# Performance work log

Measured on AMD Instinct MI355X. Metric: run time of the kernel, lower is better.

## Reference

```python
import jax, jax.numpy as jnp
import numpy as np
import math

D_MODEL = 512
EXPAND = 2
D_INNER = EXPAND * D_MODEL          # 1024
HEADDIM = 16
NHEADS = D_INNER // HEADDIM         # 64
NGROUPS = 1
D_STATE = 16
D_CONV = 4
CHUNK = 256
CONV_DIM = D_INNER + 2 * NGROUPS * D_STATE      # 1056
D_IN_PROJ = 2 * D_INNER + 2 * NGROUPS * D_STATE + NHEADS  # 2144
EPS = 1e-5


def setup_inputs() -> dict:
    key = jax.random.key(0)
    ks = jax.random.split(key, 9)
    B, L = 2, 4096
    u = jax.random.normal(ks[0], (B, L, D_MODEL), dtype=jnp.float32)
    in_proj_w = jax.random.normal(ks[1], (D_IN_PROJ, D_MODEL), dtype=jnp.float32) * (1.0 / math.sqrt(D_MODEL))
    conv_w = jax.random.normal(ks[2], (CONV_DIM, D_CONV), dtype=jnp.float32) * (1.0 / math.sqrt(D_CONV))
    conv_b = jnp.zeros((CONV_DIM,), dtype=jnp.float32)
    # dt_bias = inverse-softplus of dt sampled log-uniform in [1e-3, 1e-1]
    dt = jnp.exp(jax.random.uniform(ks[3], (NHEADS,)) * (math.log(0.1) - math.log(0.001)) + math.log(0.001))
    dt_bias = dt + jnp.log(-jnp.expm1(-dt))
    A_log = jnp.log(jax.random.uniform(ks[4], (NHEADS,), minval=1.0, maxval=16.0))
    D_skip = jnp.ones((NHEADS,), dtype=jnp.float32)
    norm_w = jnp.ones((D_INNER,), dtype=jnp.float32)
    out_proj_w = jax.random.normal(ks[5], (D_MODEL, D_INNER), dtype=jnp.float32) * (1.0 / math.sqrt(D_INNER))
    return {"u": u, "in_proj_w": in_proj_w, "conv_w": conv_w, "conv_b": conv_b,
            "dt_bias": dt_bias, "A_log": A_log, "D_skip": D_skip,
            "norm_w": norm_w, "out_proj_w": out_proj_w}


def _segsum(x):
    # x: (..., T) -> (..., T, T) lower-triangular cumulative segment sums
    T = x.shape[-1]
    cs = jnp.cumsum(x, axis=-1)
    s = cs[..., :, None] - cs[..., None, :]
    mask = jnp.tril(jnp.ones((T, T), dtype=bool))
    return jnp.where(mask, s, -jnp.inf)


def _ssd(xdt, dA, Bm, Cm):
    # xdt: (b,l,h,p) already multiplied by dt; dA: (b,l,h); Bm,Cm: (b,l,h,n)
    b, l, h, p = xdt.shape
    n = Bm.shape[-1]
    nc = l // CHUNK
    xr = xdt.reshape(b, nc, CHUNK, h, p)
    Br = Bm.reshape(b, nc, CHUNK, h, n)
    Cr = Cm.reshape(b, nc, CHUNK, h, n)
    dAr = dA.reshape(b, nc, CHUNK, h).transpose(0, 3, 1, 2)  # (b,h,nc,c)
    A_cs = jnp.cumsum(dAr, axis=-1)
    # intra-chunk (diagonal blocks)
    Ldec = jnp.exp(_segsum(dAr))                              # (b,h,nc,c,c)
    Y_diag = jnp.einsum('bclhn,bcshn,bhcls,bcshp->bclhp', Cr, Br, Ldec, xr)
    # per-chunk final states
    decay_states = jnp.exp(A_cs[..., -1:] - A_cs)             # (b,h,nc,c)
    states = jnp.einsum('bclhn,bhcl,bclhp->bchpn', Br, decay_states, xr)
    states = jnp.concatenate([jnp.zeros_like(states[:, :1]), states], axis=1)
    chunk_sums = jnp.pad(A_cs[..., -1], ((0, 0), (0, 0), (1, 0)))  # (b,h,nc+1)
    decay_chunk = jnp.exp(_segsum(chunk_sums))                # (b,h,nc+1,nc+1)
    new_states = jnp.einsum('bhzc,bchpn->bzhpn', decay_chunk, states)
    prev_states = new_states[:, :-1]                          # (b,nc,h,p,n)
    # inter-chunk contribution
    state_decay_out = jnp.exp(A_cs)                           # (b,h,nc,c)
    Y_off = jnp.einsum('bclhn,bchpn,bhcl->bclhp', Cr, prev_states, state_decay_out)
    return (Y_diag + Y_off).reshape(b, l, h, p)


def _forward(u, in_proj_w, conv_w, conv_b, dt_bias, A_log, D_skip, norm_w, out_proj_w):
    b, l, _ = u.shape
    zxbcdt = jnp.einsum('bld,ed->ble', u, in_proj_w)
    z = zxbcdt[..., :D_INNER]
    xBC = zxbcdt[..., D_INNER:D_INNER + CONV_DIM]
    dt = zxbcdt[..., D_INNER + CONV_DIM:]
    dt = jax.nn.softplus(dt + dt_bias)                        # (b,l,h)
    # causal depthwise conv1d + silu
    xBC_t = xBC.transpose(0, 2, 1)                            # (b, conv_dim, l)
    conv_out = jax.lax.conv_general_dilated(
        xBC_t, conv_w[:, None, :], window_strides=(1,),
        padding=[(D_CONV - 1, 0)], feature_group_count=CONV_DIM,
        dimension_numbers=('NCH', 'OIH', 'NCH'))
    xBC = jax.nn.silu((conv_out + conv_b[None, :, None]).transpose(0, 2, 1))
    x = xBC[..., :D_INNER].reshape(b, l, NHEADS, HEADDIM)
    Bg = xBC[..., D_INNER:D_INNER + NGROUPS * D_STATE].reshape(b, l, NGROUPS, D_STATE)
    Cg = xBC[..., D_INNER + NGROUPS * D_STATE:].reshape(b, l, NGROUPS, D_STATE)
    hpg = NHEADS // NGROUPS
    Bm = jnp.repeat(Bg, hpg, axis=2)                          # (b,l,h,n)
    Cm = jnp.repeat(Cg, hpg, axis=2)
    A = -jnp.exp(A_log)                                       # (h,)
    dA = dt * A                                               # (b,l,h)
    y = _ssd(x * dt[..., None], dA, Bm, Cm)
    y = y + x * D_skip[None, None, :, None]
    y = y.reshape(b, l, D_INNER)
    # gated RMSNorm (norm_before_gate=False): norm(y * silu(z)) * w
    y = y * jax.nn.silu(z)
    y = y * jax.lax.rsqrt(jnp.mean(y * y, axis=-1, keepdims=True) + EPS) * norm_w
    return jnp.einsum('ble,de->bld', y, out_proj_w)


def reference(u, in_proj_w, conv_w, conv_b, dt_bias, A_log, D_skip, norm_w, out_proj_w):
    return _forward(u, in_proj_w, conv_w, conv_b, dt_bias, A_log, D_skip, norm_w, out_proj_w)
```

## Files before the change

kernel.cpp:

```cpp
#include <hip/hip_runtime.h>
#include <hip/hip_bf16.h>
#include <math.h>

#define D_MODEL   512
#define D_INNER   1024
#define NHEADS    64
#define HEADDIM   16
#define D_STATE   16
#define CONV_DIM  1056
#define D_IN_PROJ 2144
#define CHUNK     256
#define NCHUNK    16
#define BATCH     2
#define SEQ       4096
#define ROWS      (BATCH * SEQ)
#define LDZX      2176

typedef __bf16    bf16x8 __attribute__((ext_vector_type(8)));
typedef _Float16  f16x8  __attribute__((ext_vector_type(8)));
typedef float     f32x4  __attribute__((ext_vector_type(4)));
typedef float     f32x16 __attribute__((ext_vector_type(16)));
typedef unsigned short u16x8 __attribute__((ext_vector_type(8)));
typedef unsigned int   u32x4 __attribute__((ext_vector_type(4)));

__device__ __forceinline__ float softplusf(float x) {
    return (x > 20.f) ? x : log1pf(expf(x));
}
__device__ __forceinline__ float siluf(float x) {
    return x / (1.f + expf(-x));
}
__device__ __forceinline__ unsigned short f2b(float x) {
    union { __hip_bfloat16 h; unsigned short u; } cv;
    cv.h = __float2bfloat16(x);
    return cv.u;
}
__device__ __forceinline__ float b2f(unsigned short u) {
    union { float f; unsigned int i; } c;
    c.i = (unsigned int)u << 16;
    return c.f;
}
__device__ __forceinline__ void load_lds16(const unsigned short* g, unsigned short* l) {
    __builtin_amdgcn_global_load_lds(
        (const __attribute__((address_space(1))) void*)g,
        (__attribute__((address_space(3))) void*)l,
        16, 0, 0);
}

__global__ __launch_bounds__(256) void cast_all(const float* __restrict__ u,
                                                const float* __restrict__ Win,
                                                const float* __restrict__ Wout,
                                                unsigned short* __restrict__ u_bf,
                                                unsigned short* __restrict__ win_bf,
                                                unsigned short* __restrict__ wout_bf) {
    const int bid = blockIdx.x;
    u16x8 o;
    if (bid < 2048) {
        const int i = (bid * 256 + threadIdx.x) * 8;
        float4 a = *(const float4*)(u + i);
        float4 b = *(const float4*)(u + i + 4);
        o[0] = f2b(a.x); o[1] = f2b(a.y); o[2] = f2b(a.z); o[3] = f2b(a.w);
        o[4] = f2b(b.x); o[5] = f2b(b.y); o[6] = f2b(b.z); o[7] = f2b(b.w);
        *(u16x8*)(u_bf + i) = o;
    } else if (bid < 2592) {
        const int i = ((bid - 2048) * 256 + threadIdx.x) * 8;
        const int n = 2144 * 512;
        if (i + 8 <= n) {
            float4 a = *(const float4*)(Win + i);
            float4 b = *(const float4*)(Win + i + 4);
            o[0] = f2b(a.x); o[1] = f2b(a.y); o[2] = f2b(a.z); o[3] = f2b(a.w);
            o[4] = f2b(b.x); o[5] = f2b(b.y); o[6] = f2b(b.z); o[7] = f2b(b.w);
        } else {
            #pragma unroll
            for (int j = 0; j < 8; ++j) o[j] = (i + j < n) ? f2b(Win[i + j]) : (unsigned short)0;
        }
        *(u16x8*)(win_bf + i) = o;
    } else {
        const int i = ((bid - 2592) * 256 + threadIdx.x) * 8;
        float4 a = *(const float4*)(Wout + i);
        float4 b = *(const float4*)(Wout + i + 4);
        o[0] = f2b(a.x); o[1] = f2b(a.y); o[2] = f2b(a.z); o[3] = f2b(a.w);
        o[4] = f2b(b.x); o[5] = f2b(b.y); o[6] = f2b(b.z); o[7] = f2b(b.w);
        *(u16x8*)(wout_bf + i) = o;
    }
}

__global__ __launch_bounds__(256) void gemm_in(const unsigned short* __restrict__ A,
                                               const unsigned short* __restrict__ B,
                                               unsigned short* __restrict__ C16,
                                               float* __restrict__ dtsp,
                                               const float* __restrict__ dtb) {
    __shared__ unsigned short smem[32768];
    const int t    = threadIdx.x;
    const int wave = t >> 6;
    const int lane = t & 63;
    const int bid  = blockIdx.x;
    const int swz  = (bid & 7) * 136 + (bid >> 3);
    const int by   = swz / 17;
    const int bx   = swz - by * 17;
    const int bm   = by * 128;
    const int bn   = bx * 128;
    const int wr   = wave >> 1;
    const int wc   = wave & 1;

    const int fr = lane & 15;
    const int kb = (lane >> 4) * 8;

    f32x4 acc[4][4] = {};

    auto stage = [&](int it) {
        const int k0 = it * 64;
        unsigned short* dst = smem + (it & 1) * 16384;
        #pragma unroll
        for (int q = 0; q < 4; ++q) {
            const int p = q * 256 + t;
            const int r = p >> 3;
            const int sl = (p & 7) ^ (r & 7);
            load_lds16(A + (size_t)(bm + r) * 512 + k0 + sl * 8, dst + p * 8);
        }
        #pragma unroll
        for (int q = 0; q < 4; ++q) {
            const int p = q * 256 + t;
            const int r = p >> 3;
            const int sl = (p & 7) ^ (r & 7);
            load_lds16(B + (size_t)(bn + r) * 512 + k0 + sl * 8, dst + 8192 + p * 8);
        }
    };

    stage(0);
    __syncthreads();

    for (int it = 0; it < 8; ++it) {
        if (it + 1 < 8) stage(it + 1);
        const unsigned short* Ab = smem + (it & 1) * 16384;
        const unsigned short* Bb = Ab + 8192;
        #pragma unroll
        for (int kk = 0; kk < 2; ++kk) {
            const int c0 = kk * 32 + kb;
            const int s0 = c0 >> 3;
            bf16x8 af[4], bfr[4];
            #pragma unroll
            for (int m = 0; m < 4; ++m) {
                const int R = wr * 64 + m * 16 + fr;
                af[m] = *reinterpret_cast<const bf16x8*>(&Ab[R * 64 + ((s0 ^ (R & 7)) << 3)]);
            }
            #pragma unroll
            for (int n = 0; n < 4; ++n) {
                const int R = wc * 64 + n * 16 + fr;
                bfr[n] = *reinterpret_cast<const bf16x8*>(&Bb[R * 64 + ((s0 ^ (R & 7)) << 3)]);
            }
            #pragma unroll
            for (int m = 0; m < 4; ++m)
                #pragma unroll
                for (int n = 0; n < 4; ++n)
                    acc[m][n] = __builtin_amdgcn_mfma_f32_16x16x32_bf16(af[m], bfr[n], acc[m][n], 0, 0, 0);
        }
        __syncthreads();
    }

    if (bn == 2048) {
        #pragma unroll
        for (int m = 0; m < 4; ++m) {
            #pragma unroll
            for (int n = 0; n < 4; ++n) {
                const int col = bn + wc * 64 + fr + n * 16;
                if (col >= 2080 && col < 2144) {
                    const int h = col - 2080;
                    const float bias = dtb[h];
                    #pragma unroll
                    for (int j = 0; j < 4; ++j) {
                        const int row = bm + wr * 64 + ((lane >> 4) << 2) + m * 16 + j;
                        dtsp[(size_t)row * 64 + h] = softplusf(acc[m][n][j] + bias);
                    }
                }
            }
        }
    }
    #pragma unroll
    for (int m = 0; m < 4; ++m) {
        #pragma unroll
        for (int n = 0; n < 4; ++n) {
            const int lcol = wc * 64 + fr + n * 16;
            #pragma unroll
            for (int j = 0; j < 4; ++j) {
                const int lrow = wr * 64 + ((lane >> 4) << 2) + m * 16 + j;
                smem[lrow * 128 + lcol] = f2b(acc[m][n][j]);
            }
        }
    }
    __syncthreads();
    #pragma unroll
    for (int p = 0; p < 8; ++p) {
        const int r = p * 16 + (t >> 4);
        const int cl = (t & 15) * 8;
        u16x8 v = *(const u16x8*)&smem[r * 128 + cl];
        *(u16x8*)(C16 + (size_t)(bm + r) * LDZX + bn + cl) = v;
    }
}

__global__ __launch_bounds__(256) void gemm_out(const unsigned short* __restrict__ A,
                                                const unsigned short* __restrict__ B,
                                                float* __restrict__ C) {
    __shared__ unsigned short smem[24576];
    const int t    = threadIdx.x;
    const int wave = t >> 6;
    const int lane = t & 63;
    const int bm   = blockIdx.y * 128;
    const int bn   = blockIdx.x * 64;
    const int wr   = wave >> 1;
    const int wc   = wave & 1;

    const int fr = lane & 15;
    const int kb = (lane >> 4) * 8;

    f32x4 acc[4][2] = {};

    auto stage = [&](int it) {
        const int k0 = it * 64;
        unsigned short* dst = smem + (it & 1) * 12288;
        #pragma unroll
        for (int q = 0; q < 4; ++q) {
            const int p = q * 256 + t;
            const int r = p >> 3;
            const int sl = (p & 7) ^ (r & 7);
            load_lds16(A + (size_t)(bm + r) * 1024 + k0 + sl * 8, dst + p * 8);
        }
        #pragma unroll
        for (int q = 0; q < 2; ++q) {
            const int p = q * 256 + t;
            const int r = p >> 3;
            const int sl = (p & 7) ^ (r & 7);
            load_lds16(B + (size_t)(bn + r) * 1024 + k0 + sl * 8, dst + 8192 + p * 8);
        }
    };

    stage(0);
    __syncthreads();

    for (int it = 0; it < 16; ++it) {
        if (it + 1 < 16) stage(it + 1);
        const unsigned short* Ab = smem + (it & 1) * 12288;
        const unsigned short* Bb = Ab + 8192;
        #pragma unroll
        for (int kk = 0; kk < 2; ++kk) {
            const int c0 = kk * 32 + kb;
            const int s0 = c0 >> 3;
            bf16x8 af[4], bfr[2];
            #pragma unroll
            for (int m = 0; m < 4; ++m) {
                const int R = wr * 64 + m * 16 + fr;
                af[m] = *reinterpret_cast<const bf16x8*>(&Ab[R * 64 + ((s0 ^ (R & 7)) << 3)]);
            }
            #pragma unroll
            for (int n = 0; n < 2; ++n) {
                const int R = wc * 32 + n * 16 + fr;
                bfr[n] = *reinterpret_cast<const bf16x8*>(&Bb[R * 64 + ((s0 ^ (R & 7)) << 3)]);
            }
            #pragma unroll
            for (int m = 0; m < 4; ++m)
                #pragma unroll
                for (int n = 0; n < 2; ++n)
                    acc[m][n] = __builtin_amdgcn_mfma_f32_16x16x32_bf16(af[m], bfr[n], acc[m][n], 0, 0, 0);
        }
        __syncthreads();
    }

    const int cr0 = bm + wr * 64 + ((lane >> 4) << 2);
    const int cc0 = bn + wc * 32 + fr;
    #pragma unroll
    for (int m = 0; m < 4; ++m)
        #pragma unroll
        for (int n = 0; n < 2; ++n)
            #pragma unroll
            for (int j = 0; j < 4; ++j)
                C[(size_t)(cr0 + m * 16 + j) * 512 + cc0 + n * 16] = acc[m][n][j];
}

__global__ void conv_silu44(const unsigned short* __restrict__ zxb, const float* __restrict__ cw,
                            const float* __restrict__ cb, unsigned short* __restrict__ xcb) {
    int idx = blockIdx.x * blockDim.x + threadIdx.x;
    if (idx >= (ROWS / 4) * (CONV_DIM / 4)) return;
    const int cq  = idx % (CONV_DIM / 4);
    const int blq = idx / (CONV_DIM / 4);
    const int bl0 = blq * 4;
    const int l0  = bl0 % SEQ;
    const int c4  = cq * 4;
    const unsigned short* base = zxb + (size_t)bl0 * LDZX + D_INNER + c4;
    float4 w0 = *(const float4*)(cw + (c4 + 0) * 4);
    float4 w1 = *(const float4*)(cw + (c4 + 1) * 4);
    float4 w2 = *(const float4*)(cw + (c4 + 2) * 4);
    float4 w3 = *(const float4*)(cw + (c4 + 3) * 4);
    float4 bb = *(const float4*)(cb + c4);
    float4 in[7];
    #pragma unroll
    for (int k = 0; k < 7; ++k) {
        const int off = k - 3;
        if (l0 == 0 && k < 3) {
            in[k] = make_float4(0.f, 0.f, 0.f, 0.f);
        } else {
            ushort4 uu = *(const ushort4*)(base + (long)off * LDZX);
            in[k] = make_float4(b2f(uu.x), b2f(uu.y), b2f(uu.z), b2f(uu.w));
        }
    }
    #pragma unroll
    for (int r = 0; r < 4; ++r) {
        ushort4 o;
        o.x = f2b(siluf(bb.x + w0.x * in[r].x + w0.y * in[r + 1].x + w0.z * in[r + 2].x + w0.w * in[r + 3].x));
        o.y = f2b(siluf(bb.y + w1.x * in[r].y + w1.y * in[r + 1].y + w1.z * in[r + 2].y + w1.w * in[r + 3].y));
        o.z = f2b(siluf(bb.z + w2.x * in[r].z + w2.y * in[r + 1].z + w2.z * in[r + 2].z + w2.w * in[r + 3].z));
        o.w = f2b(siluf(bb.w + w3.x * in[r].w + w3.y * in[r + 1].w + w3.z * in[r + 2].w + w3.w * in[r + 3].w));
        *(ushort4*)(xcb + (size_t)(bl0 + r) * CONV_DIM + c4) = o;
    }
}

__global__ __launch_bounds__(256, 4) void ssd_chunk(const unsigned short* __restrict__ xcb,
                                                    const float* __restrict__ dtsp,
                                                    const float* __restrict__ A_log,
                                                    unsigned short* __restrict__ ypre16,
                                                    float* __restrict__ states,
                                                    float* __restrict__ csb,
                                                    float* __restrict__ csum) {
    __shared__ _Float16 Bb[256][16];
    __shared__ _Float16 Cb[256][16];
    __shared__ _Float16 Xt[16][264];
    __shared__ _Float16 Bt[16][264];
    __shared__ float csL[256];
    __shared__ __align__(16) _Float16 decL[256];
    __shared__ float wsumL[4];

    const int bid = blockIdx.x;
    const int h = bid & 63;
    const int c = (bid >> 6) & 15;
    const int b = bid >> 10;
    const int t = threadIdx.x;
    const int wv = t >> 6;
    const int lane = t & 63;
    const int fr = lane & 15;
    const int hi = lane >> 4;
    const int l31 = lane & 31;
    const int hi5 = lane >> 5;
    const int row = b * SEQ + c * CHUNK + t;

    float Ah  = -__expf(A_log[h]);
    float dtv = dtsp[(size_t)row * NHEADS + h];
    float val = dtv * Ah;
    #pragma unroll
    for (int off = 1; off < 64; off <<= 1) {
        float o = __shfl_up(val, off, 64);
        if (lane >= off) val += o;
    }
    if (lane == 63) wsumL[wv] = val;
    __syncthreads();
    float pre = 0.f, cl = 0.f;
    #pragma unroll
    for (int w2 = 0; w2 < 4; ++w2) {
        float s = wsumL[w2];
        if (w2 < wv) pre += s;
        cl += s;
    }
    float cst = val + pre;
    csL[t] = cst;
    csb[(size_t)bid * 256 + t] = cst;
    if (t == 0) csum[(b * 64 + h) * 16 + c] = cl;
    decL[t] = (_Float16)__expf(cl - cst);

    const unsigned short* xrow = xcb + (size_t)row * CONV_DIM;
    u16x8 braw0 = *(const u16x8*)(xrow + D_INNER);
    u16x8 braw1 = *(const u16x8*)(xrow + D_INNER + 8);
    u16x8 craw0 = *(const u16x8*)(xrow + D_INNER + D_STATE);
    u16x8 craw1 = *(const u16x8*)(xrow + D_INNER + D_STATE + 8);
    u16x8 xraw0 = *(const u16x8*)(xrow + h * HEADDIM);
    u16x8 xraw1 = *(const u16x8*)(xrow + h * HEADDIM + 8);
    float bv[16], cv[16], xv[16];
    #pragma unroll
    for (int n = 0; n < 8; ++n) {
        bv[n] = b2f(braw0[n]); bv[8 + n] = b2f(braw1[n]);
        cv[n] = b2f(craw0[n]); cv[8 + n] = b2f(craw1[n]);
        xv[n] = b2f(xraw0[n]); xv[8 + n] = b2f(xraw1[n]);
    }
    {
        f16x8 pk;
        #pragma unroll
        for (int n = 0; n < 8; ++n) pk[n] = (_Float16)cv[n];
        *(f16x8*)&Cb[t][0] = pk;
        #pragma unroll
        for (int n = 0; n < 8; ++n) pk[n] = (_Float16)cv[8 + n];
        *(f16x8*)&Cb[t][8] = pk;
        #pragma unroll
        for (int n = 0; n < 8; ++n) pk[n] = (_Float16)bv[n];
        *(f16x8*)&Bb[t][0] = pk;
        #pragma unroll
        for (int n = 0; n < 8; ++n) pk[n] = (_Float16)bv[8 + n];
        *(f16x8*)&Bb[t][8] = pk;
    }
    #pragma unroll
    for (int n = 0; n < 16; ++n) {
        Bt[n][t] = (_Float16)bv[n];
        Xt[n][t] = (_Float16)(xv[n] * dtv);
    }
    __syncthreads();

    const int browbase = b * SEQ + c * CHUNK;
    const f32x16 z16 = {};

    #pragma unroll
    for (int halfi = 0; halfi < 2; ++halfi) {
        const int rt = (halfi == 0) ? wv : 7 - wv;
        const int t0 = rt * 32;
        const float cs_t = csL[t0 + l31];
        const f16x8 cfrag = *(const f16x8*)&Cb[t0 + l31][hi5 * 8];
        f32x16 yacc = {};
        for (int sb = 0; sb <= rt; ++sb) {
            const int s0 = sb * 32;
            f16x8 bfrag = *(const f16x8*)&Bb[s0 + l31][hi5 * 8];
            f32x16 sp = __builtin_amdgcn_mfma_f32_32x32x16_f16(bfrag, cfrag, z16, 0, 0, 0);
            const bool diag = (sb == rt);
            unsigned int D[8];
            #pragma unroll
            for (int j = 0; j < 8; ++j) {
                const int q0 = 2 * j;
                const int sr0 = (q0 & 3) + 8 * (q0 >> 2) + 4 * hi5;
                float p0 = sp[q0] * __expf(cs_t - csL[s0 + sr0]);
                float p1 = sp[q0 + 1] * __expf(cs_t - csL[s0 + sr0 + 1]);
                if (diag) {
                    p0 = (sr0 <= l31) ? p0 : 0.f;
                    p1 = (sr0 + 1 <= l31) ? p1 : 0.f;
                }
                D[j] = __builtin_bit_cast(unsigned int, __builtin_amdgcn_cvt_pkrtz(p0, p1));
            }
            unsigned int pD[8];
            #pragma unroll
            for (int j = 0; j < 8; ++j) pD[j] = (unsigned int)__shfl_xor((int)D[j], 32, 64);
            u32x4 fa;
            fa[0] = hi5 ? pD[2] : D[0];
            fa[1] = hi5 ? pD[3] : D[1];
            fa[2] = hi5 ? D[2] : pD[0];
            fa[3] = hi5 ? D[3] : pD[1];
            f16x8 pf0 = __builtin_bit_cast(f16x8, fa);
            f16x8 xf0 = *(const f16x8*)&Xt[fr][s0 + hi5 * 8];
            yacc = __builtin_amdgcn_mfma_f32_32x32x16_f16(pf0, xf0, yacc, 0, 0, 0);
            fa[0] = hi5 ? pD[6] : D[4];
            fa[1] = hi5 ? pD[7] : D[5];
            fa[2] = hi5 ? D[6] : pD[4];
            fa[3] = hi5 ? D[7] : pD[5];
            f16x8 pf1 = __builtin_bit_cast(f16x8, fa);
            f16x8 xf1 = *(const f16x8*)&Xt[fr][s0 + 16 + hi5 * 8];
            yacc = __builtin_amdgcn_mfma_f32_32x32x16_f16(pf1, xf1, yacc, 0, 0, 0);
        }
        if (l31 < 16) {
            #pragma unroll
            for (int q = 0; q < 16; ++q) {
                const int tr = t0 + (q & 3) + 8 * (q >> 2) + 4 * hi5;
                ypre16[(size_t)(browbase + tr) * D_INNER + h * HEADDIM + l31] = f2b(yacc[q]);
            }
        }
    }

    __syncthreads();
    float* stpart = (float*)&Cb[0][0];
    const int r0w = wv * 64;
    f32x4 stacc = {};
    #pragma unroll
    for (int kt = 0; kt < 2; ++kt) {
        const int sbase = r0w + kt * 32 + hi * 8;
        f16x8 xa = *(const f16x8*)&Xt[fr][sbase];
        f16x8 dd = *(const f16x8*)&decL[sbase];
        xa = xa * dd;
        f16x8 bb2 = *(const f16x8*)&Bt[fr][sbase];
        stacc = __builtin_amdgcn_mfma_f32_16x16x32_f16(xa, bb2, stacc, 0, 0, 0);
    }
    #pragma unroll
    for (int j = 0; j < 4; ++j)
        stpart[wv * 256 + (hi * 4 + j) * 16 + fr] = stacc[j];
    __syncthreads();
    {
        const int p = t >> 4, n = t & 15;
        float st = stpart[0 * 256 + p * 16 + n] + stpart[1 * 256 + p * 16 + n]
                 + stpart[2 * 256 + p * 16 + n] + stpart[3 * 256 + p * 16 + n];
        states[(size_t)bid * 256 + t] = st;
    }
}

__global__ __launch_bounds__(256) void ssd_rec(const float* __restrict__ states,
                                               const float* __restrict__ csum,
                                               float* __restrict__ prevst) {
    __shared__ float dec[16];
    const int bh = blockIdx.x;
    const int b = bh >> 6, h = bh & 63;
    const int t = threadIdx.x;
    if (t < 16) dec[t] = __expf(csum[bh * 16 + t]);
    float sv[16];
    #pragma unroll
    for (int c = 0; c < NCHUNK; ++c)
        sv[c] = states[((size_t)((b * 16 + c) * 64 + h)) * 256 + t];
    __syncthreads();
    float run = 0.f;
    #pragma unroll
    for (int c = 0; c < NCHUNK; ++c) {
        prevst[((size_t)((b * 16 + c) * 64 + h)) * 256 + t] = run;
        run = run * dec[c] + sv[c];
    }
}

__global__ __launch_bounds__(512, 4) void ssd_off_norm(const unsigned short* __restrict__ xcb,
                                                       const unsigned short* __restrict__ zxb,
                                                       const unsigned short* __restrict__ ypre16,
                                                       const float* __restrict__ prevst,
                                                       const float* __restrict__ csb,
                                                       const float* __restrict__ Dskip,
                                                       const float* __restrict__ normw,
                                                       unsigned short* __restrict__ yout) {
    __shared__ float Cs[16][16];
    __shared__ float csS[64][16];
    __shared__ float nw[1024];
    __shared__ float Dn[64];
    __shared__ float red[16][8];

    const int blk = blockIdx.x;
    const int bc = blk >> 4;
    const int rb = blk & 15;
    const int r0 = rb * 16;
    const int b = bc >> 4, c = bc & 15;
    const int brow0 = b * SEQ + c * CHUNK;
    const int t = threadIdx.x;
    const int ch0 = t * 2;
    const int h = ch0 >> 4;
    const int p0 = ch0 & 15;
    const int wv = t >> 6;
    const int lane = t & 63;

    if (t < 256) *(float4*)&nw[t * 4] = *(const float4*)(normw + t * 4);
    else if (t < 320) Dn[t - 256] = Dskip[t - 256];
    if (t < 64) {
        int r = t >> 2, n4 = (t & 3) * 4;
        ushort4 uu = *(const ushort4*)(xcb + (size_t)(brow0 + r0 + r) * CONV_DIM
                                       + D_INNER + D_STATE + n4);
        Cs[r][n4 + 0] = b2f(uu.x); Cs[r][n4 + 1] = b2f(uu.y);
        Cs[r][n4 + 2] = b2f(uu.z); Cs[r][n4 + 3] = b2f(uu.w);
    }
    #pragma unroll
    for (int i = t; i < 1024; i += 512) {
        int r = i & 15, hh = i >> 4;
        csS[hh][r] = csb[(size_t)(bc * 64 + hh) * 256 + r0 + r];
    }

    float ps[2][16];
    {
        const float* pbase = prevst + (size_t)(bc * 64 + h) * 256 + p0 * 16;
        #pragma unroll
        for (int n4 = 0; n4 < 16; n4 += 4) {
            *(float4*)&ps[0][n4] = *(const float4*)(pbase + n4);
            *(float4*)&ps[1][n4] = *(const float4*)(pbase + 16 + n4);
        }
    }
    __syncthreads();

    const float d = Dn[h];
    const float nw0 = nw[ch0], nw1 = nw[ch0 + 1];

    float g0r[16], g1r[16];
    #pragma unroll
    for (int r = 0; r < 16; ++r) {
        const size_t grow = (size_t)(brow0 + r0 + r);
        ushort2 yu = *(const ushort2*)(ypre16 + grow * D_INNER + ch0);
        ushort2 xu = *(const ushort2*)(xcb + grow * CONV_DIM + ch0);
        ushort2 zu = *(const ushort2*)(zxb + grow * LDZX + ch0);
        float sdo = __expf(csS[h][r]);
        float off0 = 0.f, off1 = 0.f;
        #pragma unroll
        for (int n = 0; n < 16; ++n) {
            float cn = Cs[r][n];
            off0 += cn * ps[0][n];
            off1 += cn * ps[1][n];
        }
        float g0 = (b2f(yu.x) + sdo * off0 + b2f(xu.x) * d) * siluf(b2f(zu.x));
        float g1 = (b2f(yu.y) + sdo * off1 + b2f(xu.y) * d) * siluf(b2f(zu.y));
        g0r[r] = g0; g1r[r] = g1;
        float s = g0 * g0 + g1 * g1;
        #pragma unroll
        for (int o = 32; o > 0; o >>= 1) s += __shfl_down(s, o, 64);
        if (lane == 0) red[r][wv] = s;
    }
    __syncthreads();
    #pragma unroll
    for (int r = 0; r < 16; ++r) {
        const size_t grow = (size_t)(brow0 + r0 + r);
        float tot = 0.f;
        #pragma unroll
        for (int w2 = 0; w2 < 8; ++w2) tot += red[r][w2];
        float rstd = rsqrtf(tot * (1.f / (float)D_INNER) + 1e-5f);
        ushort2 o2;
        o2.x = f2b(g0r[r] * rstd * nw0);
        o2.y = f2b(g1r[r] * rstd * nw1);
        *(ushort2*)(yout + grow * D_INNER + ch0) = o2;
    }
}

extern "C" void kernel_launch(void* const* d_in, const int* in_sizes, int n_in,
                              void* d_out, int out_size, void* d_ws, size_t ws_size,
                              hipStream_t stream) {
    const float* u     = (const float*)d_in[0];
    const float* Win   = (const float*)d_in[1];
    const float* cw    = (const float*)d_in[2];
    const float* cb    = (const float*)d_in[3];
    const float* dtb   = (const float*)d_in[4];
    const float* Alog  = (const float*)d_in[5];
    const float* Dsk   = (const float*)d_in[6];
    const float* normw = (const float*)d_in[7];
    const float* Wout  = (const float*)d_in[8];
    float* out = (float*)d_out;

    float* ws = (float*)d_ws;
    unsigned short* zxb = (unsigned short*)ws;
    float* dtsp   = ws + 8912896;
    float* csb    = dtsp + 524288;
    float* st     = csb + 524288;
    float* pst    = st + 524288;
    float* csum   = pst + 524288;
    unsigned short* ypre16 = (unsigned short*)(csum + 2048);
    unsigned short* xcb    = (unsigned short*)((float*)ypre16 + 4194304);
    unsigned short* yn_bf  = (unsigned short*)((float*)xcb + 4325376);
    unsigned short* u_bf   = (unsigned short*)((float*)yn_bf + 2097152);
    unsigned short* win_bf  = (unsigned short*)((float*)u_bf + 2097152);
    unsigned short* wout_bf = (unsigned short*)((float*)win_bf + 557056);

    cast_all<<<2848, 256, 0, stream>>>(u, Win, Wout, u_bf, win_bf, wout_bf);

    gemm_in<<<1088, 256, 0, stream>>>(u_bf, win_bf, zxb, dtsp, dtb);

    conv_silu44<<<(ROWS / 4) * (CONV_DIM / 4) / 256, 256, 0, stream>>>(zxb, cw, cb, xcb);
    ssd_chunk<<<BATCH * NCHUNK * NHEADS, 256, 0, stream>>>(xcb, dtsp, Alog, ypre16, st, csb, csum);
    ssd_rec<<<BATCH * NHEADS, 256, 0, stream>>>(st, csum, pst);
    ssd_off_norm<<<512, 512, 0, stream>>>(xcb, zxb, ypre16, pst, csb, Dsk, normw, yn_bf);

    gemm_out<<<dim3(8, 64), 256, 0, stream>>>(yn_bf, wout_bf, out);
}
```

Before: 144.7 us.

## Shrink gemm_in N-tile to 64 and restage gemm_out with 32-wide K tiles

```diff
diff --git a/kernel.cpp b/kernel.cpp
--- a/kernel.cpp
+++ b/kernel.cpp
@@ -89,27 +89,27 @@
                                                unsigned short* __restrict__ C16,
                                                float* __restrict__ dtsp,
                                                const float* __restrict__ dtb) {
-    __shared__ unsigned short smem[32768];
+    __shared__ unsigned short smem[24576];
     const int t    = threadIdx.x;
     const int wave = t >> 6;
     const int lane = t & 63;
     const int bid  = blockIdx.x;
-    const int swz  = (bid & 7) * 136 + (bid >> 3);
-    const int by   = swz / 17;
-    const int bx   = swz - by * 17;
+    const int swz  = (bid & 7) * 272 + (bid >> 3);
+    const int by   = swz / 34;
+    const int bx   = swz - by * 34;
     const int bm   = by * 128;
-    const int bn   = bx * 128;
+    const int bn   = bx * 64;
     const int wr   = wave >> 1;
     const int wc   = wave & 1;
 
     const int fr = lane & 15;
     const int kb = (lane >> 4) * 8;
 
-    f32x4 acc[4][4] = {};
+    f32x4 acc[4][2] = {};
 
     auto stage = [&](int it) {
         const int k0 = it * 64;
-        unsigned short* dst = smem + (it & 1) * 16384;
+        unsigned short* dst = smem + (it & 1) * 12288;
         #pragma unroll
         for (int q = 0; q < 4; ++q) {
             const int p = q * 256 + t;
@@ -118,7 +118,7 @@
             load_lds16(A + (size_t)(bm + r) * 512 + k0 + sl * 8, dst + p * 8);
         }
         #pragma unroll
-        for (int q = 0; q < 4; ++q) {
+        for (int q = 0; q < 2; ++q) {
             const int p = q * 256 + t;
             const int r = p >> 3;
             const int sl = (p & 7) ^ (r & 7);
@@ -131,38 +131,37 @@
 
     for (int it = 0; it < 8; ++it) {
         if (it + 1 < 8) stage(it + 1);
-        const unsigned short* Ab = smem + (it & 1) * 16384;
+        const unsigned short* Ab = smem + (it & 1) * 12288;
         const unsigned short* Bb = Ab + 8192;
         #pragma unroll
         for (int kk = 0; kk < 2; ++kk) {
-            const int c0 = kk * 32 + kb;
-            const int s0 = c0 >> 3;
-            bf16x8 af[4], bfr[4];
+            const int s0 = (kk * 32 + kb) >> 3;
+            bf16x8 af[4], bfr[2];
             #pragma unroll
             for (int m = 0; m < 4; ++m) {
                 const int R = wr * 64 + m * 16 + fr;
                 af[m] = *reinterpret_cast<const bf16x8*>(&Ab[R * 64 + ((s0 ^ (R & 7)) << 3)]);
             }
             #pragma unroll
-            for (int n = 0; n < 4; ++n) {
-                const int R = wc * 64 + n * 16 + fr;
+            for (int n = 0; n < 2; ++n) {
+                const int R = wc * 32 + n * 16 + fr;
                 bfr[n] = *reinterpret_cast<const bf16x8*>(&Bb[R * 64 + ((s0 ^ (R & 7)) << 3)]);
             }
             #pragma unroll
             for (int m = 0; m < 4; ++m)
                 #pragma unroll
-                for (int n = 0; n < 4; ++n)
+                for (int n = 0; n < 2; ++n)
                     acc[m][n] = __builtin_amdgcn_mfma_f32_16x16x32_bf16(af[m], bfr[n], acc[m][n], 0, 0, 0);
         }
         __syncthreads();
     }
 
-    if (bn == 2048) {
+    if (bn == 2048 || bn == 2112) {
         #pragma unroll
         for (int m = 0; m < 4; ++m) {
             #pragma unroll
-            for (int n = 0; n < 4; ++n) {
-                const int col = bn + wc * 64 + fr + n * 16;
+            for (int n = 0; n < 2; ++n) {
+                const int col = bn + wc * 32 + fr + n * 16;
                 if (col >= 2080 && col < 2144) {
                     const int h = col - 2080;
                     const float bias = dtb[h];
@@ -178,21 +177,22 @@
     #pragma unroll
     for (int m = 0; m < 4; ++m) {
         #pragma unroll
-        for (int n = 0; n < 4; ++n) {
-            const int lcol = wc * 64 + fr + n * 16;
+        for (int n = 0; n < 2; ++n) {
+            const int lcol = wc * 32 + fr + n * 16;
             #pragma unroll
             for (int j = 0; j < 4; ++j) {
                 const int lrow = wr * 64 + ((lane >> 4) << 2) + m * 16 + j;
-                smem[lrow * 128 + lcol] = f2b(acc[m][n][j]);
+                smem[lrow * 72 + lcol] = f2b(acc[m][n][j]);
             }
         }
     }
     __syncthreads();
     #pragma unroll
-    for (int p = 0; p < 8; ++p) {
-        const int r = p * 16 + (t >> 4);
-        const int cl = (t & 15) * 8;
-        u16x8 v = *(const u16x8*)&smem[r * 128 + cl];
+    for (int q = 0; q < 4; ++q) {
+        const int idx = q * 256 + t;
+        const int r = idx >> 3;
+        const int cl = (idx & 7) * 8;
+        u16x8 v = *(const u16x8*)&smem[r * 72 + cl];
         *(u16x8*)(C16 + (size_t)(bm + r) * LDZX + bn + cl) = v;
     }
 }
@@ -200,7 +200,7 @@
 __global__ __launch_bounds__(256) void gemm_out(const unsigned short* __restrict__ A,
                                                 const unsigned short* __restrict__ B,
                                                 float* __restrict__ C) {
-    __shared__ unsigned short smem[24576];
+    __shared__ unsigned short smem[12288];
     const int t    = threadIdx.x;
     const int wave = t >> 6;
     const int lane = t & 63;
@@ -209,59 +209,47 @@
     const int wr   = wave >> 1;
     const int wc   = wave & 1;
 
+    const int srow = wave * 16 + (lane >> 2);
+    const int scol = (lane & 3) * 8;
+    const unsigned short* ga0 = A + (size_t)(bm + srow) * 1024 + scol;
+    const unsigned short* ga1 = A + (size_t)(bm + 64 + srow) * 1024 + scol;
+    const unsigned short* gb0 = B + (size_t)(bn + srow) * 1024 + scol;
+
     const int fr = lane & 15;
     const int kb = (lane >> 4) * 8;
 
     f32x4 acc[4][2] = {};
 
-    auto stage = [&](int it) {
-        const int k0 = it * 64;
-        unsigned short* dst = smem + (it & 1) * 12288;
-        #pragma unroll
-        for (int q = 0; q < 4; ++q) {
-            const int p = q * 256 + t;
-            const int r = p >> 3;
-            const int sl = (p & 7) ^ (r & 7);
-            load_lds16(A + (size_t)(bm + r) * 1024 + k0 + sl * 8, dst + p * 8);
-        }
-        #pragma unroll
-        for (int q = 0; q < 2; ++q) {
-            const int p = q * 256 + t;
-            const int r = p >> 3;
-            const int sl = (p & 7) ^ (r & 7);
-            load_lds16(B + (size_t)(bn + r) * 1024 + k0 + sl * 8, dst + 8192 + p * 8);
-        }
-    };
-
-    stage(0);
-    __syncthreads();
-
-    for (int it = 0; it < 16; ++it) {
-        if (it + 1 < 16) stage(it + 1);
-        const unsigned short* Ab = smem + (it & 1) * 12288;
-        const unsigned short* Bb = Ab + 8192;
-        #pragma unroll
-        for (int kk = 0; kk < 2; ++kk) {
-            const int c0 = kk * 32 + kb;
-            const int s0 = c0 >> 3;
-            bf16x8 af[4], bfr[2];
-            #pragma unroll
-            for (int m = 0; m < 4; ++m) {
-                const int R = wr * 64 + m * 16 + fr;
-                af[m] = *reinterpret_cast<const bf16x8*>(&Ab[R * 64 + ((s0 ^ (R & 7)) << 3)]);
-            }
-            #pragma unroll
-            for (int n = 0; n < 2; ++n) {
-                const int R = wc * 32 + n * 16 + fr;
-                bfr[n] = *reinterpret_cast<const bf16x8*>(&Bb[R * 64 + ((s0 ^ (R & 7)) << 3)]);
-            }
-            #pragma unroll
-            for (int m = 0; m < 4; ++m)
-                #pragma unroll
-                for (int n = 0; n < 2; ++n)
-                    acc[m][n] = __builtin_amdgcn_mfma_f32_16x16x32_bf16(af[m], bfr[n], acc[m][n], 0, 0, 0);
-        }
+    load_lds16(ga0, smem + wave * 512);
+    load_lds16(ga1, smem + 2048 + wave * 512);
+    load_lds16(gb0, smem + 8192 + wave * 512);
+    __syncthreads();
+
+    int cur = 0;
+    for (int it = 0; it < 32; ++it) {
+        if (it + 1 < 32) {
+            const int k0 = (it + 1) * 32;
+            const int nb = cur ^ 1;
+            load_lds16(ga0 + k0, smem + nb * 4096 + wave * 512);
+            load_lds16(ga1 + k0, smem + nb * 4096 + 2048 + wave * 512);
+            load_lds16(gb0 + k0, smem + 8192 + nb * 2048 + wave * 512);
+        }
+        const unsigned short* Ab = smem + cur * 4096;
+        const unsigned short* Bb = smem + 8192 + cur * 2048;
+        bf16x8 af[4], bfr[2];
+        #pragma unroll
+        for (int m = 0; m < 4; ++m)
+            af[m] = *reinterpret_cast<const bf16x8*>(&Ab[(wr * 64 + m * 16 + fr) * 32 + kb]);
+        #pragma unroll
+        for (int n = 0; n < 2; ++n)
+            bfr[n] = *reinterpret_cast<const bf16x8*>(&Bb[(wc * 32 + n * 16 + fr) * 32 + kb]);
+        #pragma unroll
+        for (int m = 0; m < 4; ++m)
+            #pragma unroll
+            for (int n = 0; n < 2; ++n)
+                acc[m][n] = __builtin_amdgcn_mfma_f32_16x16x32_bf16(af[m], bfr[n], acc[m][n], 0, 0, 0);
         __syncthreads();
+        cur ^= 1;
     }
 
     const int cr0 = bm + wr * 64 + ((lane >> 4) << 2);
@@ -625,7 +613,7 @@
 
     cast_all<<<2848, 256, 0, stream>>>(u, Win, Wout, u_bf, win_bf, wout_bf);
 
-    gemm_in<<<1088, 256, 0, stream>>>(u_bf, win_bf, zxb, dtsp, dtb);
+    gemm_in<<<2176, 256, 0, stream>>>(u_bf, win_bf, zxb, dtsp, dtb);
 
     conv_silu44<<<(ROWS / 4) * (CONV_DIM / 4) / 256, 256, 0, stream>>>(zxb, cw, cb, xcb);
     ssd_chunk<<<BATCH * NCHUNK * NHEADS, 256, 0, stream>>>(xcb, dtsp, Alog, ypre16, st, csb, csum);
```

After: 142.6 us, median of 2. No clear change (-1.5%).
